# Performance work log

Hardware: AMD Instinct MI355X
Metric: run time of the kernel (lower is better)

The kernel has to match this reference:

```python
import jax, jax.numpy as jnp
import numpy as np

IMAGE_SIZE = 320
SIGMA = 0.01      # soft-edge width in NDC units (~1.6 px at 320 res)
CHUNK = 128       # faces per scan step (bounds peak memory)


def setup_inputs() -> dict:
    key = jax.random.key(0)
    k1, k2 = jax.random.split(key)
    verts = jax.random.normal(k1, (4, 778, 3), dtype=jnp.float32) * 0.5
    faces = jax.random.randint(k2, (1538, 3), 0, 778, dtype=jnp.int32)
    return {"verts": verts, "faces": faces}


def _silhouette(verts, faces):
    B = verts.shape[0]
    S = IMAGE_SIZE
    # NMR.forward flips the y axis of verts before rendering
    v = verts * jnp.array([1.0, -1.0, 1.0], dtype=verts.dtype)
    xy = v[..., :2]  # orthographic projection (perspective=False)
    F = faces.shape[0]
    n_chunks = -(-F // CHUNK)
    Fp = n_chunks * CHUNK
    faces_p = jnp.pad(faces, ((0, Fp - F), (0, 0)))
    valid = (jnp.arange(Fp) < F).astype(verts.dtype)
    tri = xy[:, faces_p]  # [B, Fp, 3, 2]
    tri = jnp.moveaxis(tri.reshape(B, n_chunks, CHUNK, 3, 2), 1, 0)  # [nc,B,C,3,2]
    valid = valid.reshape(n_chunks, CHUNK)
    # pixel centers in NDC [-1, 1]
    lin = (jnp.arange(S, dtype=verts.dtype) + 0.5) / S * 2.0 - 1.0
    py, px = jnp.meshgrid(lin, lin, indexing="ij")
    px = px.reshape(-1)  # [P]
    py = py.reshape(-1)

    def edge_d(a, b, sgn):
        # signed distance of every pixel to oriented edge a->b: [B, C, P]
        ex = b[..., 0] - a[..., 0]
        ey = b[..., 1] - a[..., 1]
        inv_len = 1.0 / (jnp.sqrt(ex * ex + ey * ey) + 1e-8)
        d = (ex[..., None] * (py[None, None, :] - a[..., 1:2])
             - ey[..., None] * (px[None, None, :] - a[..., 0:1]))
        return sgn[..., None] * d * inv_len[..., None]

    def body(acc, chunk):
        tri_c, m = chunk  # [B,C,3,2], [C]
        v0, v1, v2 = tri_c[..., 0, :], tri_c[..., 1, :], tri_c[..., 2, :]
        # orientation sign so CW / CCW triangles are handled uniformly
        area2 = ((v1[..., 0] - v0[..., 0]) * (v2[..., 1] - v0[..., 1])
                 - (v1[..., 1] - v0[..., 1]) * (v2[..., 0] - v0[..., 0]))
        sgn = jnp.sign(area2)
        logp = (jax.nn.log_sigmoid(edge_d(v0, v1, sgn) / SIGMA)
                + jax.nn.log_sigmoid(edge_d(v1, v2, sgn) / SIGMA)
                + jax.nn.log_sigmoid(edge_d(v2, v0, sgn) / SIGMA))
        prob = jnp.clip(jnp.exp(logp) * m[None, :, None], 0.0, 1.0 - 1e-6)
        return acc + jnp.sum(jnp.log1p(-prob), axis=1), None

    acc0 = jnp.zeros((B, S * S), dtype=verts.dtype)
    acc, _ = jax.lax.scan(body, acc0, (tri, valid))
    # silhouette = 1 - prod_f (1 - coverage_f), accumulated in log space
    return (1.0 - jnp.exp(acc)).reshape(B, S, S)


def reference(verts, faces):
    return _silhouette(verts, faces)
```

## Files before the change

### kernel.cpp

```cpp
#include <hip/hip_runtime.h>
#include <math.h>


#define IMG_S 320
#define N_FACES 1538
#define N_VERTS 778
#define N_BATCH 4
#define FP 1600
#define TILE 8
#define CHUNK_F 768
#define MAXB 772
#define NWAVE 4
#define INV_SIGMA 100.0f
#define T_CUT 12.0f
#define ACC_CUT_P 2.2603294e-6f
#define LOG2_1EM6 -19.9315686f

__global__ __launch_bounds__(256)
void prep_faces(const float* __restrict__ verts,
                const int* __restrict__ faces,
                float4* __restrict__ gE0,
                float4* __restrict__ gE1,
                float4* __restrict__ gE2)
{
    const int f = blockIdx.x * 256 + threadIdx.x;
    const int b = blockIdx.z;
    if (f >= N_FACES) return;

    const float* vb = verts + (size_t)b * N_VERTS * 3;
    const int i0 = faces[f * 3 + 0];
    const int i1 = faces[f * 3 + 1];
    const int i2 = faces[f * 3 + 2];
    const float x0 = vb[i0 * 3 + 0], y0 = -vb[i0 * 3 + 1];
    const float x1 = vb[i1 * 3 + 0], y1 = -vb[i1 * 3 + 1];
    const float x2 = vb[i2 * 3 + 0], y2 = -vb[i2 * 3 + 1];

    const float dx1 = x1 - x0, dy1 = y1 - y0;
    const float dx2 = x2 - x0, dy2 = y2 - y0;
    const float area2 = __builtin_fmaf(dx1, dy2, -__fmul_rn(dy1, dx2));
    const float sgn = (area2 > 0.0f) ? 1.0f : ((area2 < 0.0f) ? -1.0f : 0.0f);

    const size_t o = (size_t)b * FP + f;
    {
        const float ex = x1 - x0, ey = y1 - y0;
        const float s = sgn * INV_SIGMA / (sqrtf(ex * ex + ey * ey) + 1e-8f);
        gE0[o] = make_float4(-s * ey, s * ex, s * (ey * x0 - ex * y0), 0.0f);
    }
    {
        const float ex = x2 - x1, ey = y2 - y1;
        const float s = sgn * INV_SIGMA / (sqrtf(ex * ex + ey * ey) + 1e-8f);
        gE1[o] = make_float4(-s * ey, s * ex, s * (ey * x1 - ex * y1), 0.0f);
    }
    {
        const float ex = x0 - x2, ey = y0 - y2;
        const float s = sgn * INV_SIGMA / (sqrtf(ex * ex + ey * ey) + 1e-8f);
        gE2[o] = make_float4(-s * ey, s * ex, s * (ey * x2 - ex * y2), 0.0f);
    }
}

__global__ __launch_bounds__(256)
void silhouette_ws(const float4* __restrict__ gE0,
                   const float4* __restrict__ gE1,
                   const float4* __restrict__ gE2,
                   float* __restrict__ out)
{
    __shared__ float4 sE0[MAXB];
    __shared__ float4 sE1[MAXB];
    __shared__ float4 sE2[MAXB];
    __shared__ float sAcc[256];
    __shared__ int sCount;
    __shared__ int sAlive;
    __shared__ int sCover;

    const int t    = threadIdx.x;
    const int wave = t >> 6;
    const int lane = t & 63;
    const int p    = t & 63;
    const int plx  = p & 7;
    const int ply  = p >> 3;
    const int b    = blockIdx.z;
    const int gx   = blockIdx.x * TILE + plx;
    const int gy   = blockIdx.y * TILE + ply;

    const float w  = 2.0f / IMG_S;
    const float px = (gx + 0.5f) * w - 1.0f;
    const float py = (gy + 0.5f) * w - 1.0f;
    const float cx = (blockIdx.x * TILE + 4) * w - 1.0f;
    const float cy = (blockIdx.y * TILE + 4) * w - 1.0f;
    const float rr = 3.5f * w;

    const float4* gb0 = gE0 + (size_t)b * FP;
    const float4* gb1 = gE1 + (size_t)b * FP;
    const float4* gb2 = gE2 + (size_t)b * FP;

    float acc = 1.0f;

    for (int c = 0; c < 2; ++c) {
        const int base = c * CHUNK_F;
        const int end  = (c == 0) ? CHUNK_F : N_FACES;

        sAcc[t] = acc;
        if (t == 0) { sCount = 0; sAlive = 0; sCover = 0; }
        __syncthreads();

        const float tot = sAcc[p] * sAcc[p + 64] * sAcc[p + 128] * sAcc[p + 192];
        const bool alive = (tot > ACC_CUT_P);
        if (alive) sAlive = 1;
        __syncthreads();

        if (sAlive == 0) break;

        for (int fb = base; fb < end; fb += 256) {
            const int fc = fb + t;
            const bool vald = (fc < end);
            const int fcc = vald ? fc : (end - 1);
            const float4 e0 = gb0[fcc];
            const float4 e1 = gb1[fcc];
            const float4 e2 = gb2[fcc];
            const float c0 = fmaf(e0.x, cx, fmaf(e0.y, cy, e0.z));
            const float c1 = fmaf(e1.x, cx, fmaf(e1.y, cy, e1.z));
            const float c2 = fmaf(e2.x, cx, fmaf(e2.y, cy, e2.z));
            const float r0 = rr * (fabsf(e0.x) + fabsf(e0.y));
            const float r1 = rr * (fabsf(e1.x) + fabsf(e1.y));
            const float r2 = rr * (fabsf(e2.x) + fabsf(e2.y));
            const float m_hi = fminf(c0 + r0, fminf(c1 + r1, c2 + r2));
            const float m_lo = fminf(c0 - r0, fminf(c1 - r1, c2 - r2));
            const bool isCov  = vald && (m_lo > T_CUT);
            const bool isBand = vald && !isCov && (m_hi > -T_CUT);

            const unsigned long long mb = __ballot(isBand);
            int wbase = 0;
            if (lane == 0) {
                const int nw = __popcll(mb);
                if (nw) wbase = atomicAdd(&sCount, nw);
            }
            wbase = __shfl(wbase, 0);
            if (isBand) {
                const int pos = wbase + __popcll(mb & ((1ull << lane) - 1ull));
                sE0[pos] = e0;
                sE1[pos] = e1;
                sE2[pos] = e2;
            }
            const unsigned long long mc = __ballot(isCov);
            if (lane == 0) {
                const int ncv = __popcll(mc);
                if (ncv) atomicAdd(&sCover, ncv);
            }
        }
        __syncthreads();

        const float coverF = exp2f((float)sCover * LOG2_1EM6);
        bool live = alive && (acc * coverF > ACC_CUT_P);
        if (wave == 0) acc *= coverF;

        const int n = sCount;
        int j = wave;
        while (j < n) {
            if (__ballot(live) == 0ull) break;
            const int j1 = j + NWAVE;
            const int j1c = (j1 < n) ? j1 : j;
            const float4 A0 = sE0[j],   A1 = sE1[j],   A2 = sE2[j];
            const float4 B0 = sE0[j1c], B1 = sE1[j1c], B2 = sE2[j1c];
            {
                const float xa = fmaf(A0.x, px, fmaf(A0.y, py, A0.z));
                const float xb = fmaf(A1.x, px, fmaf(A1.y, py, A1.z));
                const float xc = fmaf(A2.x, px, fmaf(A2.y, py, A2.z));
                const float m = fminf(xa, fminf(xb, xc));
                if (live && m > -T_CUT) {
                    const float da = 1.0f + __expf(-xa);
                    const float db = 1.0f + __expf(-xb);
                    const float dc = 1.0f + __expf(-xc);
                    const float f = fmaxf(
                        1.0f - __builtin_amdgcn_rcpf(da * db * dc), 1e-6f);
                    acc *= f;
                    live = (acc > ACC_CUT_P);
                }
            }
            if (j1 < n) {
                const float xa = fmaf(B0.x, px, fmaf(B0.y, py, B0.z));
                const float xb = fmaf(B1.x, px, fmaf(B1.y, py, B1.z));
                const float xc = fmaf(B2.x, px, fmaf(B2.y, py, B2.z));
                const float m = fminf(xa, fminf(xb, xc));
                if (live && m > -T_CUT) {
                    const float da = 1.0f + __expf(-xa);
                    const float db = 1.0f + __expf(-xb);
                    const float dc = 1.0f + __expf(-xc);
                    const float f = fmaxf(
                        1.0f - __builtin_amdgcn_rcpf(da * db * dc), 1e-6f);
                    acc *= f;
                    live = (acc > ACC_CUT_P);
                }
            }
            j += 2 * NWAVE;
        }
    }

    sAcc[t] = acc;
    __syncthreads();
    if (t < 64) {
        const float tot = sAcc[p] * sAcc[p + 64] * sAcc[p + 128] * sAcc[p + 192];
        out[(size_t)b * (IMG_S * IMG_S) + (size_t)gy * IMG_S + gx] = 1.0f - tot;
    }
}

extern "C" void kernel_launch(void* const* d_in, const int* in_sizes, int n_in,
                              void* d_out, int out_size, void* d_ws, size_t ws_size,
                              hipStream_t stream) {
    const float* verts = (const float*)d_in[0];
    const int* faces = (const int*)d_in[1];
    float* out = (float*)d_out;

    float4* gE0 = (float4*)d_ws;
    float4* gE1 = gE0 + (size_t)N_BATCH * FP;
    float4* gE2 = gE1 + (size_t)N_BATCH * FP;

    dim3 pgrid((N_FACES + 255) / 256, 1, N_BATCH);
    prep_faces<<<pgrid, 256, 0, stream>>>(verts, faces, gE0, gE1, gE2);

    dim3 grid(IMG_S / TILE, IMG_S / TILE, N_BATCH);
    silhouette_ws<<<grid, 256, 0, stream>>>(gE0, gE1, gE2, out);
}
```

Measured before the change: 88.36 us.

## Bin faces into per-tile lists in a separate kernel before rasterization

Adds a bin_faces kernel that computes each face's conservative screen bounding box from its edge equations and, for each overlapping 8x8 tile, either counts it as fully covering or appends it to that tile's global band list via atomics. The raster kernel then loads only its tile's band faces, in chunks of 384, instead of having every block scan all 1538 faces. This removes the redundant per-block culling pass over every face. In exchange it adds a kernel launch, global atomics and a roughly 40MB list buffer, plus extra workspace. List order is now nondeterministic, so float accumulation order varies between runs.

```diff
diff --git a/kernel.cpp b/kernel.cpp
--- a/kernel.cpp
+++ b/kernel.cpp
@@ -3,26 +3,33 @@
 
 
 #define IMG_S 320
+#define N_TILES 40
 #define N_FACES 1538
 #define N_VERTS 778
 #define N_BATCH 4
 #define FP 1600
 #define TILE 8
-#define CHUNK_F 768
-#define MAXB 772
+#define MAXB 384
+#define LIST_STRIDE 1600
 #define NWAVE 4
 #define INV_SIGMA 100.0f
 #define T_CUT 12.0f
 #define ACC_CUT_P 2.2603294e-6f
 #define LOG2_1EM6 -19.9315686f
+#define N_BINS (N_BATCH * N_TILES * N_TILES)
 
 __global__ __launch_bounds__(256)
 void prep_faces(const float* __restrict__ verts,
                 const int* __restrict__ faces,
                 float4* __restrict__ gE0,
                 float4* __restrict__ gE1,
-                float4* __restrict__ gE2)
+                float4* __restrict__ gE2,
+                int* __restrict__ cnts)
 {
+    const int g = (blockIdx.z * gridDim.x + blockIdx.x) * 256 + threadIdx.x;
+    const int nthr = gridDim.x * gridDim.z * 256;
+    for (int i = g; i < 2 * N_BINS; i += nthr) cnts[i] = 0;
+
     const int f = blockIdx.x * 256 + threadIdx.x;
     const int b = blockIdx.z;
     if (f >= N_FACES) return;
@@ -59,22 +66,122 @@
 }
 
 __global__ __launch_bounds__(256)
+void bin_faces(const float4* __restrict__ gE0,
+               const float4* __restrict__ gE1,
+               const float4* __restrict__ gE2,
+               int* __restrict__ bandCnt,
+               int* __restrict__ coverCnt,
+               int* __restrict__ list)
+{
+    const int t    = threadIdx.x;
+    const int wave = t >> 6;
+    const int lane = t & 63;
+    const int f    = blockIdx.x * 4 + wave;
+    const int b    = blockIdx.z;
+    if (f >= N_FACES) return;
+
+    const size_t o = (size_t)b * FP + f;
+    const float4 e0 = gE0[o];
+    const float4 e1 = gE1[o];
+    const float4 e2 = gE2[o];
+
+    const float pw = 2.0f / IMG_S;
+    const float rr = 3.5f * pw;
+    const float r0 = rr * (fabsf(e0.x) + fabsf(e0.y));
+    const float r1 = rr * (fabsf(e1.x) + fabsf(e1.y));
+    const float r2 = rr * (fabsf(e2.x) + fabsf(e2.y));
+
+    const float C0 = e0.z + T_CUT + r0 + 0.5f;
+    const float C1 = e1.z + T_CUT + r1 + 0.5f;
+    const float C2 = e2.z + T_CUT + r2 + 0.5f;
+
+    float xmn = 1e30f, xmx = -1e30f, ymn = 1e30f, ymx = -1e30f;
+    bool ok = true;
+    {
+        const float w = e0.x * e1.y - e0.y * e1.x;
+        if (fabsf(w) < 1e-3f) ok = false;
+        else {
+            const float iw = 1.0f / w;
+            const float x = (e0.y * C1 - C0 * e1.y) * iw;
+            const float y = (C0 * e1.x - e0.x * C1) * iw;
+            xmn = fminf(xmn, x); xmx = fmaxf(xmx, x);
+            ymn = fminf(ymn, y); ymx = fmaxf(ymx, y);
+        }
+    }
+    {
+        const float w = e1.x * e2.y - e1.y * e2.x;
+        if (fabsf(w) < 1e-3f) ok = false;
+        else {
+            const float iw = 1.0f / w;
+            const float x = (e1.y * C2 - C1 * e2.y) * iw;
+            const float y = (C1 * e2.x - e1.x * C2) * iw;
+            xmn = fminf(xmn, x); xmx = fmaxf(xmx, x);
+            ymn = fminf(ymn, y); ymx = fmaxf(ymx, y);
+        }
+    }
+    {
+        const float w = e2.x * e0.y - e2.y * e0.x;
+        if (fabsf(w) < 1e-3f) ok = false;
+        else {
+            const float iw = 1.0f / w;
+            const float x = (e2.y * C0 - C2 * e0.y) * iw;
+            const float y = (C2 * e0.x - e2.x * C0) * iw;
+            xmn = fminf(xmn, x); xmx = fmaxf(xmx, x);
+            ymn = fminf(ymn, y); ymx = fmaxf(ymx, y);
+        }
+    }
+    if (!ok || !(xmn <= xmx) || !(ymn <= ymx)) {
+        xmn = -1.0f; xmx = 1.0f; ymn = -1.0f; ymx = 1.0f;
+    }
+    xmn = fmaxf(xmn, -1.0f); xmx = fminf(xmx, 1.0f);
+    ymn = fmaxf(ymn, -1.0f); ymx = fminf(ymx, 1.0f);
+
+    const int tx0 = max(0,  (int)floorf(((xmn + 1.0f) * 160.0f - 4.0f) * 0.125f) - 1);
+    const int tx1 = min(N_TILES - 1, (int)ceilf(((xmx + 1.0f) * 160.0f - 4.0f) * 0.125f) + 1);
+    const int ty0 = max(0,  (int)floorf(((ymn + 1.0f) * 160.0f - 4.0f) * 0.125f) - 1);
+    const int ty1 = min(N_TILES - 1, (int)ceilf(((ymx + 1.0f) * 160.0f - 4.0f) * 0.125f) + 1);
+    const int nx = tx1 - tx0 + 1;
+    const int ny = ty1 - ty0 + 1;
+    if (nx <= 0 || ny <= 0) return;
+    const int ntile = nx * ny;
+
+    for (int k = lane; k < ntile; k += 64) {
+        const int tx = tx0 + k % nx;
+        const int ty = ty0 + k / nx;
+        const float cxx = (tx * TILE + 4) * pw - 1.0f;
+        const float cyy = (ty * TILE + 4) * pw - 1.0f;
+        const float c0 = fmaf(e0.x, cxx, fmaf(e0.y, cyy, e0.z));
+        const float c1 = fmaf(e1.x, cxx, fmaf(e1.y, cyy, e1.z));
+        const float c2 = fmaf(e2.x, cxx, fmaf(e2.y, cyy, e2.z));
+        const float m_hi = fminf(c0 + r0, fminf(c1 + r1, c2 + r2));
+        const float m_lo = fminf(c0 - r0, fminf(c1 - r1, c2 - r2));
+        const int tid = (b * N_TILES + ty) * N_TILES + tx;
+        if (m_lo > T_CUT) {
+            atomicAdd(&coverCnt[tid], 1);
+        } else if (m_hi > -T_CUT) {
+            const int s = atomicAdd(&bandCnt[tid], 1);
+            list[(size_t)tid * LIST_STRIDE + s] = f;
+        }
+    }
+}
+
+__global__ __launch_bounds__(256)
 void silhouette_ws(const float4* __restrict__ gE0,
                    const float4* __restrict__ gE1,
                    const float4* __restrict__ gE2,
+                   const int* __restrict__ bandCnt,
+                   const int* __restrict__ coverCnt,
+                   const int* __restrict__ list,
                    float* __restrict__ out)
 {
     __shared__ float4 sE0[MAXB];
     __shared__ float4 sE1[MAXB];
     __shared__ float4 sE2[MAXB];
     __shared__ float sAcc[256];
-    __shared__ int sCount;
     __shared__ int sAlive;
-    __shared__ int sCover;
 
     const int t    = threadIdx.x;
     const int wave = t >> 6;
-    const int lane = t & 63;
     const int p    = t & 63;
     const int plx  = p & 7;
     const int ply  = p >> 3;
@@ -85,80 +192,44 @@
     const float w  = 2.0f / IMG_S;
     const float px = (gx + 0.5f) * w - 1.0f;
     const float py = (gy + 0.5f) * w - 1.0f;
-    const float cx = (blockIdx.x * TILE + 4) * w - 1.0f;
-    const float cy = (blockIdx.y * TILE + 4) * w - 1.0f;
-    const float rr = 3.5f * w;
 
     const float4* gb0 = gE0 + (size_t)b * FP;
     const float4* gb1 = gE1 + (size_t)b * FP;
     const float4* gb2 = gE2 + (size_t)b * FP;
 
-    float acc = 1.0f;
-
-    for (int c = 0; c < 2; ++c) {
-        const int base = c * CHUNK_F;
-        const int end  = (c == 0) ? CHUNK_F : N_FACES;
+    const int tid = (b * N_TILES + blockIdx.y) * N_TILES + blockIdx.x;
+    const int n   = bandCnt[tid];
+    const int cov = coverCnt[tid];
+    const int* myList = list + (size_t)tid * LIST_STRIDE;
+
+    float acc = (wave == 0) ? exp2f((float)cov * LOG2_1EM6) : 1.0f;
+
+    for (int base = 0; base < n; base += MAXB) {
+        const int nn = min(MAXB, n - base);
 
         sAcc[t] = acc;
-        if (t == 0) { sCount = 0; sAlive = 0; sCover = 0; }
+        if (t == 0) sAlive = 0;
         __syncthreads();
-
         const float tot = sAcc[p] * sAcc[p + 64] * sAcc[p + 128] * sAcc[p + 192];
         const bool alive = (tot > ACC_CUT_P);
         if (alive) sAlive = 1;
         __syncthreads();
-
         if (sAlive == 0) break;
 
-        for (int fb = base; fb < end; fb += 256) {
-            const int fc = fb + t;
-            const bool vald = (fc < end);
-            const int fcc = vald ? fc : (end - 1);
-            const float4 e0 = gb0[fcc];
-            const float4 e1 = gb1[fcc];
-            const float4 e2 = gb2[fcc];
-            const float c0 = fmaf(e0.x, cx, fmaf(e0.y, cy, e0.z));
-            const float c1 = fmaf(e1.x, cx, fmaf(e1.y, cy, e1.z));
-            const float c2 = fmaf(e2.x, cx, fmaf(e2.y, cy, e2.z));
-            const float r0 = rr * (fabsf(e0.x) + fabsf(e0.y));
-            const float r1 = rr * (fabsf(e1.x) + fabsf(e1.y));
-            const float r2 = rr * (fabsf(e2.x) + fabsf(e2.y));
-            const float m_hi = fminf(c0 + r0, fminf(c1 + r1, c2 + r2));
-            const float m_lo = fminf(c0 - r0, fminf(c1 - r1, c2 - r2));
-            const bool isCov  = vald && (m_lo > T_CUT);
-            const bool isBand = vald && !isCov && (m_hi > -T_CUT);
-
-            const unsigned long long mb = __ballot(isBand);
-            int wbase = 0;
-            if (lane == 0) {
-                const int nw = __popcll(mb);
-                if (nw) wbase = atomicAdd(&sCount, nw);
-            }
-            wbase = __shfl(wbase, 0);
-            if (isBand) {
-                const int pos = wbase + __popcll(mb & ((1ull << lane) - 1ull));
-                sE0[pos] = e0;
-                sE1[pos] = e1;
-                sE2[pos] = e2;
-            }
-            const unsigned long long mc = __ballot(isCov);
-            if (lane == 0) {
-                const int ncv = __popcll(mc);
-                if (ncv) atomicAdd(&sCover, ncv);
-            }
+        for (int k = t; k < nn; k += 256) {
+            const int idx = myList[base + k];
+            sE0[k] = gb0[idx];
+            sE1[k] = gb1[idx];
+            sE2[k] = gb2[idx];
         }
         __syncthreads();
 
-        const float coverF = exp2f((float)sCover * LOG2_1EM6);
-        bool live = alive && (acc * coverF > ACC_CUT_P);
-        if (wave == 0) acc *= coverF;
-
-        const int n = sCount;
+        bool live = alive && (acc > ACC_CUT_P);
         int j = wave;
-        while (j < n) {
+        while (j < nn) {
             if (__ballot(live) == 0ull) break;
             const int j1 = j + NWAVE;
-            const int j1c = (j1 < n) ? j1 : j;
+            const int j1c = (j1 < nn) ? j1 : j;
             const float4 A0 = sE0[j],   A1 = sE1[j],   A2 = sE2[j];
             const float4 B0 = sE0[j1c], B1 = sE1[j1c], B2 = sE2[j1c];
             {
@@ -176,7 +247,7 @@
                     live = (acc > ACC_CUT_P);
                 }
             }
-            if (j1 < n) {
+            if (j1 < nn) {
                 const float xa = fmaf(B0.x, px, fmaf(B0.y, py, B0.z));
                 const float xb = fmaf(B1.x, px, fmaf(B1.y, py, B1.z));
                 const float xc = fmaf(B2.x, px, fmaf(B2.y, py, B2.z));
@@ -213,10 +284,17 @@
     float4* gE0 = (float4*)d_ws;
     float4* gE1 = gE0 + (size_t)N_BATCH * FP;
     float4* gE2 = gE1 + (size_t)N_BATCH * FP;
+    int* bandCnt  = (int*)(gE2 + (size_t)N_BATCH * FP);
+    int* coverCnt = bandCnt + N_BINS;
+    int* list     = coverCnt + N_BINS;
 
     dim3 pgrid((N_FACES + 255) / 256, 1, N_BATCH);
-    prep_faces<<<pgrid, 256, 0, stream>>>(verts, faces, gE0, gE1, gE2);
+    prep_faces<<<pgrid, 256, 0, stream>>>(verts, faces, gE0, gE1, gE2, bandCnt);
+
+    dim3 bgrid((N_FACES + 3) / 4, 1, N_BATCH);
+    bin_faces<<<bgrid, 256, 0, stream>>>(gE0, gE1, gE2, bandCnt, coverCnt, list);
 
     dim3 grid(IMG_S / TILE, IMG_S / TILE, N_BATCH);
-    silhouette_ws<<<grid, 256, 0, stream>>>(gE0, gE1, gE2, out);
+    silhouette_ws<<<grid, 256, 0, stream>>>(gE0, gE1, gE2, bandCnt, coverCnt,
+                                            list, out);
 }
```

Measured after the change: 121.0 us. 36.9% more time.

## Bin faces by per-face tile bounding box before per-tile culling

Applied to the files above, without the earlier changes.

The prep kernel now computes a conservative tile-space bounding box for each face's influence region (intersection of the offset edge half-planes) and packs it into a 32-bit word. Each tile block first scans these boxes to build a compact candidate list in shared memory, then runs the existing cull-and-shade loop only over candidates in chunks of 256. This cuts the per-tile global loads and cull tests over all faces and shrinks the shared edge buffers. In exchange it adds a prologue pass, an extra sync and more prep work, and relies on the bounding box being conservative for correctness.

```diff
diff --git a/kernel.cpp b/kernel.cpp
--- a/kernel.cpp
+++ b/kernel.cpp
@@ -3,13 +3,14 @@
 
 
 #define IMG_S 320
+#define N_TILES 40
 #define N_FACES 1538
 #define N_VERTS 778
 #define N_BATCH 4
 #define FP 1600
 #define TILE 8
-#define CHUNK_F 768
-#define MAXB 772
+#define MAXB 256
+#define MAXCAND 1544
 #define NWAVE 4
 #define INV_SIGMA 100.0f
 #define T_CUT 12.0f
@@ -21,7 +22,8 @@
                 const int* __restrict__ faces,
                 float4* __restrict__ gE0,
                 float4* __restrict__ gE1,
-                float4* __restrict__ gE2)
+                float4* __restrict__ gE2,
+                unsigned int* __restrict__ gBB)
 {
     const int f = blockIdx.x * 256 + threadIdx.x;
     const int b = blockIdx.z;
@@ -41,33 +43,98 @@
     const float sgn = (area2 > 0.0f) ? 1.0f : ((area2 < 0.0f) ? -1.0f : 0.0f);
 
     const size_t o = (size_t)b * FP + f;
+    float4 e0, e1, e2;
     {
         const float ex = x1 - x0, ey = y1 - y0;
         const float s = sgn * INV_SIGMA / (sqrtf(ex * ex + ey * ey) + 1e-8f);
-        gE0[o] = make_float4(-s * ey, s * ex, s * (ey * x0 - ex * y0), 0.0f);
+        e0 = make_float4(-s * ey, s * ex, s * (ey * x0 - ex * y0), 0.0f);
     }
     {
         const float ex = x2 - x1, ey = y2 - y1;
         const float s = sgn * INV_SIGMA / (sqrtf(ex * ex + ey * ey) + 1e-8f);
-        gE1[o] = make_float4(-s * ey, s * ex, s * (ey * x1 - ex * y1), 0.0f);
+        e1 = make_float4(-s * ey, s * ex, s * (ey * x1 - ex * y1), 0.0f);
     }
     {
         const float ex = x0 - x2, ey = y0 - y2;
         const float s = sgn * INV_SIGMA / (sqrtf(ex * ex + ey * ey) + 1e-8f);
-        gE2[o] = make_float4(-s * ey, s * ex, s * (ey * x2 - ex * y2), 0.0f);
-    }
+        e2 = make_float4(-s * ey, s * ex, s * (ey * x2 - ex * y2), 0.0f);
+    }
+    gE0[o] = e0;
+    gE1[o] = e1;
+    gE2[o] = e2;
+
+    const float pw = 2.0f / IMG_S;
+    const float rr = 3.5f * pw;
+    const float r0 = rr * (fabsf(e0.x) + fabsf(e0.y));
+    const float r1 = rr * (fabsf(e1.x) + fabsf(e1.y));
+    const float r2 = rr * (fabsf(e2.x) + fabsf(e2.y));
+    const float C0 = e0.z + T_CUT + r0 + 0.5f;
+    const float C1 = e1.z + T_CUT + r1 + 0.5f;
+    const float C2 = e2.z + T_CUT + r2 + 0.5f;
+
+    float xmn = 1e30f, xmx = -1e30f, ymn = 1e30f, ymx = -1e30f;
+    bool ok = true;
+    {
+        const float ww = e0.x * e1.y - e0.y * e1.x;
+        if (fabsf(ww) < 1e-3f) ok = false;
+        else {
+            const float iw = 1.0f / ww;
+            const float x = (e0.y * C1 - C0 * e1.y) * iw;
+            const float y = (C0 * e1.x - e0.x * C1) * iw;
+            xmn = fminf(xmn, x); xmx = fmaxf(xmx, x);
+            ymn = fminf(ymn, y); ymx = fmaxf(ymx, y);
+        }
+    }
+    {
+        const float ww = e1.x * e2.y - e1.y * e2.x;
+        if (fabsf(ww) < 1e-3f) ok = false;
+        else {
+            const float iw = 1.0f / ww;
+            const float x = (e1.y * C2 - C1 * e2.y) * iw;
+            const float y = (C1 * e2.x - e1.x * C2) * iw;
+            xmn = fminf(xmn, x); xmx = fmaxf(xmx, x);
+            ymn = fminf(ymn, y); ymx = fmaxf(ymx, y);
+        }
+    }
+    {
+        const float ww = e2.x * e0.y - e2.y * e0.x;
+        if (fabsf(ww) < 1e-3f) ok = false;
+        else {
+            const float iw = 1.0f / ww;
+            const float x = (e2.y * C0 - C2 * e0.y) * iw;
+            const float y = (C2 * e0.x - e2.x * C0) * iw;
+            xmn = fminf(xmn, x); xmx = fmaxf(xmx, x);
+            ymn = fminf(ymn, y); ymx = fmaxf(ymx, y);
+        }
+    }
+    if (!ok || !(xmn <= xmx) || !(ymn <= ymx)) {
+        xmn = -1.0f; xmx = 1.0f; ymn = -1.0f; ymx = 1.0f;
+    }
+    xmn = fmaxf(xmn, -1.0f); xmx = fminf(xmx, 1.0f);
+    ymn = fmaxf(ymn, -1.0f); ymx = fminf(ymx, 1.0f);
+
+    const int tx0 = max(0,  (int)floorf(((xmn + 1.0f) * 160.0f - 4.0f) * 0.125f) - 1);
+    const int tx1 = min(N_TILES - 1, (int)ceilf(((xmx + 1.0f) * 160.0f - 4.0f) * 0.125f) + 1);
+    const int ty0 = max(0,  (int)floorf(((ymn + 1.0f) * 160.0f - 4.0f) * 0.125f) - 1);
+    const int ty1 = min(N_TILES - 1, (int)ceilf(((ymx + 1.0f) * 160.0f - 4.0f) * 0.125f) + 1);
+
+    gBB[o] = (unsigned)tx0 | ((unsigned)max(tx1, tx0) << 8) |
+             ((unsigned)ty0 << 16) | ((unsigned)max(ty1, ty0) << 24);
 }
 
 __global__ __launch_bounds__(256)
 void silhouette_ws(const float4* __restrict__ gE0,
                    const float4* __restrict__ gE1,
                    const float4* __restrict__ gE2,
+                   const unsigned int* __restrict__ gBB,
                    float* __restrict__ out)
 {
     __shared__ float4 sE0[MAXB];
     __shared__ float4 sE1[MAXB];
     __shared__ float4 sE2[MAXB];
+    __shared__ unsigned short sCand[MAXCAND];
     __shared__ float sAcc[256];
+    __shared__ int sNC;
     __shared__ int sCount;
     __shared__ int sAlive;
     __shared__ int sCover;
@@ -79,44 +146,67 @@
     const int plx  = p & 7;
     const int ply  = p >> 3;
     const int b    = blockIdx.z;
-    const int gx   = blockIdx.x * TILE + plx;
-    const int gy   = blockIdx.y * TILE + ply;
+    const int tx   = blockIdx.x;
+    const int ty   = blockIdx.y;
+    const int gx   = tx * TILE + plx;
+    const int gy   = ty * TILE + ply;
 
     const float w  = 2.0f / IMG_S;
     const float px = (gx + 0.5f) * w - 1.0f;
     const float py = (gy + 0.5f) * w - 1.0f;
-    const float cx = (blockIdx.x * TILE + 4) * w - 1.0f;
-    const float cy = (blockIdx.y * TILE + 4) * w - 1.0f;
+    const float cx = (tx * TILE + 4) * w - 1.0f;
+    const float cy = (ty * TILE + 4) * w - 1.0f;
     const float rr = 3.5f * w;
 
     const float4* gb0 = gE0 + (size_t)b * FP;
     const float4* gb1 = gE1 + (size_t)b * FP;
     const float4* gb2 = gE2 + (size_t)b * FP;
+    const unsigned int* bbb = gBB + (size_t)b * FP;
+
+    if (t == 0) sNC = 0;
+    __syncthreads();
+    for (int fb = 0; fb < N_FACES; fb += 256) {
+        const int f = fb + t;
+        bool hit = false;
+        if (f < N_FACES) {
+            const unsigned bb = bbb[f];
+            hit = (tx >= (int)(bb & 255u))         && (tx <= (int)((bb >> 8) & 255u)) &&
+                  (ty >= (int)((bb >> 16) & 255u)) && (ty <= (int)(bb >> 24));
+        }
+        const unsigned long long mh = __ballot(hit);
+        int wb = 0;
+        if (lane == 0) {
+            const int nw = __popcll(mh);
+            if (nw) wb = atomicAdd(&sNC, nw);
+        }
+        wb = __shfl(wb, 0);
+        if (hit) sCand[wb + __popcll(mh & ((1ull << lane) - 1ull))] =
+                     (unsigned short)f;
+    }
+    __syncthreads();
+    const int nCand = sNC;
 
     float acc = 1.0f;
 
-    for (int c = 0; c < 2; ++c) {
-        const int base = c * CHUNK_F;
-        const int end  = (c == 0) ? CHUNK_F : N_FACES;
+    for (int base = 0; base < nCand; base += MAXB) {
+        const int nn2 = min(MAXB, nCand - base);
 
         sAcc[t] = acc;
         if (t == 0) { sCount = 0; sAlive = 0; sCover = 0; }
         __syncthreads();
-
         const float tot = sAcc[p] * sAcc[p + 64] * sAcc[p + 128] * sAcc[p + 192];
         const bool alive = (tot > ACC_CUT_P);
         if (alive) sAlive = 1;
         __syncthreads();
-
         if (sAlive == 0) break;
 
-        for (int fb = base; fb < end; fb += 256) {
-            const int fc = fb + t;
-            const bool vald = (fc < end);
-            const int fcc = vald ? fc : (end - 1);
-            const float4 e0 = gb0[fcc];
-            const float4 e1 = gb1[fcc];
-            const float4 e2 = gb2[fcc];
+        {
+            const int k = base + t;
+            const bool vald = (k < nCand);
+            const int fc = sCand[vald ? k : base];
+            const float4 e0 = gb0[fc];
+            const float4 e1 = gb1[fc];
+            const float4 e2 = gb2[fc];
             const float c0 = fmaf(e0.x, cx, fmaf(e0.y, cy, e0.z));
             const float c1 = fmaf(e1.x, cx, fmaf(e1.y, cy, e1.z));
             const float c2 = fmaf(e2.x, cx, fmaf(e2.y, cy, e2.z));
@@ -146,6 +236,7 @@
                 const int ncv = __popcll(mc);
                 if (ncv) atomicAdd(&sCover, ncv);
             }
+            (void)nn2;
         }
         __syncthreads();
 
@@ -213,10 +304,11 @@
     float4* gE0 = (float4*)d_ws;
     float4* gE1 = gE0 + (size_t)N_BATCH * FP;
     float4* gE2 = gE1 + (size_t)N_BATCH * FP;
+    unsigned int* gBB = (unsigned int*)(gE2 + (size_t)N_BATCH * FP);
 
     dim3 pgrid((N_FACES + 255) / 256, 1, N_BATCH);
-    prep_faces<<<pgrid, 256, 0, stream>>>(verts, faces, gE0, gE1, gE2);
+    prep_faces<<<pgrid, 256, 0, stream>>>(verts, faces, gE0, gE1, gE2, gBB);
 
     dim3 grid(IMG_S / TILE, IMG_S / TILE, N_BATCH);
-    silhouette_ws<<<grid, 256, 0, stream>>>(gE0, gE1, gE2, out);
+    silhouette_ws<<<grid, 256, 0, stream>>>(gE0, gE1, gE2, gBB, out);
 }
```

Result: faster. 85.95 us (-2.7%).
